# Optimization experiments

Measured on AMD Instinct MI355X. Metric: run time of the kernel, lower is better.

## Reference

```python
import jax, jax.numpy as jnp
import numpy as np

SEQ_LEN, IN_CH, OUT_CH, H, BATCH = 2048, 16, 1, 80, 512


def _lstm(x, W_ih, W_hh, b_ih, b_hh):
    """Single-layer batch-first LSTM (PyTorch gate order i,f,g,o).
    x: [B, T, D]. Returns (outputs [B, T, H], last hidden [B, H])."""
    B = x.shape[0]
    h0 = jnp.zeros((B, H), x.dtype)
    c0 = jnp.zeros((B, H), x.dtype)
    # Precompute input projections for all timesteps in one GEMM: [T, B, 4H]
    xproj = jnp.einsum('btd,gd->tbg', x, W_ih) + (b_ih + b_hh)

    def step(carry, xp_t):
        h, c = carry
        gates = xp_t + h @ W_hh.T  # [B, 4H]
        i, f, g, o = jnp.split(gates, 4, axis=-1)
        i = jax.nn.sigmoid(i)
        f = jax.nn.sigmoid(f)
        g = jnp.tanh(g)
        o = jax.nn.sigmoid(o)
        c = f * c + i * g
        h = o * jnp.tanh(c)
        return (h, c), h

    (h_last, _), hs = jax.lax.scan(step, (h0, c0), xproj)
    return jnp.swapaxes(hs, 0, 1), h_last


def setup_inputs() -> dict:
    key = jax.random.key(0)
    ks = jax.random.split(key, 12)
    s1 = 1.0 / np.sqrt(H)
    d = {
        'x': jax.random.normal(ks[0], (BATCH, SEQ_LEN, IN_CH), jnp.float32),
        'W_ih1': jax.random.uniform(ks[1], (4 * H, IN_CH), jnp.float32, -s1, s1),
        'W_hh1': jax.random.uniform(ks[2], (4 * H, H), jnp.float32, -s1, s1),
        'b_ih1': jax.random.uniform(ks[3], (4 * H,), jnp.float32, -s1, s1),
        'b_hh1': jax.random.uniform(ks[4], (4 * H,), jnp.float32, -s1, s1),
        'W_ih2': jax.random.uniform(ks[5], (4 * H, H), jnp.float32, -s1, s1),
        'W_hh2': jax.random.uniform(ks[6], (4 * H, H), jnp.float32, -s1, s1),
        'b_ih2': jax.random.uniform(ks[7], (4 * H,), jnp.float32, -s1, s1),
        'b_hh2': jax.random.uniform(ks[8], (4 * H,), jnp.float32, -s1, s1),
        'W_d': jax.random.uniform(ks[9], (OUT_CH, H), jnp.float32, -s1, s1),
        'b_d': jax.random.uniform(ks[10], (OUT_CH,), jnp.float32, -s1, s1),
    }
    return d


def reference(x, W_ih1, W_hh1, b_ih1, b_hh1, W_ih2, W_hh2, b_ih2, b_hh2, W_d, b_d):
    B = x.shape[0]
    x = x.reshape((B, SEQ_LEN, IN_CH))
    y1, _ = _lstm(x, W_ih1, W_hh1, b_ih1, b_hh1)          # [B, T, H]
    _, h_last = _lstm(y1, W_ih2, W_hh2, b_ih2, b_hh2)     # [B, H]
    return h_last @ W_d.T + b_d                           # [B, OUT_CH]
```

## Files before the change

### kernel.cpp

```cpp
#include <hip/hip_runtime.h>

#define T_SEQ 2048
#define DIN   16
#define HH    80
#define NTHR  512
#define NBLK  256
#define BT    2
#define ROWE  192

#define L2E   1.44269504088896340736f

typedef _Float16 f16x8 __attribute__((ext_vector_type(8)));
typedef float    f32x4 __attribute__((ext_vector_type(4)));

__device__ __forceinline__ float rcp_fast(float x){ return __builtin_amdgcn_rcpf(x); }
__device__ __forceinline__ float ex2(float x){
#if __has_builtin(__builtin_amdgcn_exp2f)
    return __builtin_amdgcn_exp2f(x);
#else
    return exp2f(x);
#endif
}

#define MF(av, bv, cv) __builtin_amdgcn_mfma_f32_16x16x32_f16(av, bv, cv, 0, 0, 0)

#define L1SLOT(acc, s) { acc = MF(A[s][0], BL0, BIAS[s]); acc = MF(A[s][1], BL1, acc); \
                         acc = MF(A[s][2], BL2, acc); }
#define L2SLOT(acc, s) { acc = MF(A[s][0], BM0, BIAS[s]); acc = MF(A[s][1], BM1, acc); \
                         acc = MF(A[s][2], BM2, acc); acc = MF(A[s][3], BM3, acc); \
                         acc = MF(A[s][4], BM4, acc); }

__global__
__attribute__((amdgpu_flat_work_group_size(NTHR, NTHR)))
__attribute__((amdgpu_waves_per_eu(2, 2)))
void lstm2_mfma(
    const float* __restrict__ x,
    const float* __restrict__ W_ih1, const float* __restrict__ W_hh1,
    const float* __restrict__ b_ih1, const float* __restrict__ b_hh1,
    const float* __restrict__ W_ih2, const float* __restrict__ W_hh2,
    const float* __restrict__ b_ih2, const float* __restrict__ b_hh2,
    const float* __restrict__ W_d,   const float* __restrict__ b_d,
    float* __restrict__ out)
{
    __shared__ __align__(16) _Float16 HB[2][BT][ROWE];

    const int t    = threadIdx.x;
    const int lane = t & 63;
    const int wv   = t >> 6;
    const int m16  = lane & 15;
    const int kgrp = lane >> 4;
    const int b0   = blockIdx.x * BT;

    const int nL1 = (wv < 4) ? 3 : 2;
    const int l1b = (wv < 4) ? 3*wv : 12 + 2*(wv-4);
    const int l2b = (wv < 4) ? 2*wv :  8 + 3*(wv-4);

    f16x8 A[5][5];
    f32x4 BIAS[5];
    {
        const int g  = m16 & 3;
        const int ut = m16 >> 2;
        const float sc = (g == 2) ? (2.f*L2E) : L2E;
        #pragma unroll
        for (int s = 0; s < 5; ++s) {
            const bool sl1 = (s < nL1);
            const int  gt  = sl1 ? (l1b + s) : (l2b + (s - nL1));
            const int  grow = g*HH + 4*gt + ut;
            #pragma unroll
            for (int c = 0; c < 5; ++c) {
                if (sl1 && c >= 3) continue;
                f16x8 a;
                #pragma unroll
                for (int j = 0; j < 8; ++j) {
                    const int k = 32*c + 8*kgrp + j;
                    const float v = sl1
                        ? ((k < DIN) ? W_ih1[grow*DIN + k] : W_hh1[grow*HH + (k - DIN)])
                        : ((k < HH)  ? W_ih2[grow*HH  + k] : W_hh2[grow*HH + (k - HH)]);
                    a[j] = (_Float16)(v * sc);
                }
                A[s][c] = a;
            }
            const int u = 4*gt + kgrp;
            const float* bI = sl1 ? b_ih1 : b_ih2;
            const float* bH = sl1 ? b_hh1 : b_hh2;
            f32x4 bb;
            bb[0] = (bI[       u] + bH[       u]) * L2E;
            bb[1] = (bI[ 80  + u] + bH[ 80  + u]) * L2E;
            bb[2] = (bI[160  + u] + bH[160  + u]) * (2.f*L2E);
            bb[3] = (bI[240  + u] + bH[240  + u]) * L2E;
            BIAS[s] = bb;
        }
    }

    const int  te      = m16 >> 1;
    const bool act_ep  = (m16 < 10);
    const int  sE      = act_ep ? te : 0;
    const bool eL1     = (sE < nL1);
    const int  gtE     = eL1 ? (l1b + sE) : (l2b + (sE - nL1));
    const int  unit_ep = 4*gtE + kgrp;
    const int  seg     = eL1 ? DIN : (DIN + HH);
    const int  batch_ep = lane & 1;

    for (int i = t; i < 2*BT*ROWE; i += NTHR) ((_Float16*)HB)[i] = (_Float16)0.f;
    __syncthreads();

    const int xbn = (lane >> 4) & 1;
    const int xch = lane & 15;
    const float* xptr = x + ((size_t)(b0 + xbn) * T_SEQ) * DIN + xch;
    float xa = 0.f, xbv = 0.f, xcv = 0.f;
    if (wv == 0 && lane < 32) {
        HB[0][xbn][xch] = (_Float16)xptr[0];
        xa  = xptr[1*DIN];
        xbv = xptr[2*DIN];
        xcv = xptr[3*DIN];
    }
    __syncthreads();

    float cst = 0.f;

    #pragma unroll 1
    for (int k = 0; k <= T_SEQ; ++k) {
        const int pb = k & 1, nb = pb ^ 1;

        if (wv == 0 && lane < 32) {
            HB[nb][xbn][xch] = (_Float16)xa;
            xa = xbv; xbv = xcv;
            const int tn = (k + 4 < T_SEQ) ? (k + 4) : (T_SEQ - 1);
            xcv = xptr[(size_t)tn * DIN];
        }

        const _Float16* rb = &HB[pb][lane & 1][0];
        const f16x8 BL0 = *(const f16x8*)(rb +       8*kgrp);
        const f16x8 BL1 = *(const f16x8*)(rb +  32 + 8*kgrp);
        const f16x8 BL2 = *(const f16x8*)(rb +  64 + 8*kgrp);
        const f16x8 BM0 = *(const f16x8*)(rb +  16 + 8*kgrp);
        const f16x8 BM1 = *(const f16x8*)(rb +  48 + 8*kgrp);
        const f16x8 BM2 = *(const f16x8*)(rb +  80 + 8*kgrp);
        const f16x8 BM3 = *(const f16x8*)(rb + 112 + 8*kgrp);
        const f16x8 BM4 = *(const f16x8*)(rb + 144 + 8*kgrp);

        f32x4 acc0, acc1, acc2, acc3, acc4;
        if (wv < 4) {
            L1SLOT(acc0, 0) L1SLOT(acc1, 1) L1SLOT(acc2, 2)
            L2SLOT(acc3, 3) L2SLOT(acc4, 4)
        } else {
            L1SLOT(acc0, 0) L1SLOT(acc1, 1)
            L2SLOT(acc2, 2) L2SLOT(acc3, 3) L2SLOT(acc4, 4)
        }

        float M0 = acc0[0], M1 = acc0[1], M2 = acc0[2], M3 = acc0[3];
        if (te == 1) { M0 = acc1[0]; M1 = acc1[1]; M2 = acc1[2]; M3 = acc1[3]; }
        if (te == 2) { M0 = acc2[0]; M1 = acc2[1]; M2 = acc2[2]; M3 = acc2[3]; }
        if (te == 3) { M0 = acc3[0]; M1 = acc3[1]; M2 = acc3[2]; M3 = acc3[3]; }
        if (te == 4) { M0 = acc4[0]; M1 = acc4[1]; M2 = acc4[2]; M3 = acc4[3]; }

        const float iv = rcp_fast(1.f + ex2(-M0));
        const float fv = rcp_fast(1.f + ex2(-M1));
        const float gv = 1.f - 2.f*rcp_fast(1.f + ex2(M2));
        const float ov = rcp_fast(1.f + ex2(-M3));
        const bool  cup = eL1 || (k > 0);
        if (cup) cst = fv*cst + iv*gv;
        const float tc = 1.f - 2.f*rcp_fast(1.f + ex2(cst * (2.f*L2E)));
        if (act_ep && cup)
            HB[nb][batch_ep][seg + unit_ep] = (_Float16)(ov * tc);

        __syncthreads();
    }

    if (wv == 0) {
        float a0 = 0.f, a1 = 0.f;
        for (int u = lane; u < HH; u += 64) {
            const float wd = W_d[u];
            a0 += wd * (float)HB[1][0][DIN + HH + u];
            a1 += wd * (float)HB[1][1][DIN + HH + u];
        }
        #pragma unroll
        for (int off = 32; off > 0; off >>= 1) {
            a0 += __shfl_down(a0, off);
            a1 += __shfl_down(a1, off);
        }
        if (lane == 0) { out[b0] = a0 + b_d[0]; out[b0 + 1] = a1 + b_d[0]; }
    }
}

extern "C" void kernel_launch(void* const* d_in, const int* in_sizes, int n_in,
                              void* d_out, int out_size, void* d_ws, size_t ws_size,
                              hipStream_t stream) {
    const float* x     = (const float*)d_in[0];
    const float* W_ih1 = (const float*)d_in[1];
    const float* W_hh1 = (const float*)d_in[2];
    const float* b_ih1 = (const float*)d_in[3];
    const float* b_hh1 = (const float*)d_in[4];
    const float* W_ih2 = (const float*)d_in[5];
    const float* W_hh2 = (const float*)d_in[6];
    const float* b_ih2 = (const float*)d_in[7];
    const float* b_hh2 = (const float*)d_in[8];
    const float* W_d   = (const float*)d_in[9];
    const float* b_d   = (const float*)d_in[10];

    lstm2_mfma<<<NBLK, NTHR, 0, stream>>>(x, W_ih1, W_hh1, b_ih1, b_hh1,
                                          W_ih2, W_hh2, b_ih2, b_hh2,
                                          W_d, b_d, (float*)d_out);
}
```

Before: 1.346 ms.

## Split layer 1 onto dot2 VALU waves and layer 2 onto MFMA waves

Layer 1 now runs on three waves using packed fp16 dot2 instructions, with two lanes per hidden unit and a DPP lane swap to combine the halves. Layer 2 runs on four MFMA-only waves, and one wave is left idle. Input x moves to its own shared buffer, so the hidden-state row shrinks and the MFMA waves no longer waste work on padded layer-1 tiles. The aim is to overlap VALU and MFMA work per step and shorten the critical path, at the cost of uneven wave load and heavy register pinning.

```diff
diff --git a/kernel.cpp b/kernel.cpp
--- a/kernel.cpp
+++ b/kernel.cpp
@@ -6,12 +6,13 @@
 #define NTHR  512
 #define NBLK  256
 #define BT    2
-#define ROWE  192
+#define ROWE  160
 
 #define L2E   1.44269504088896340736f
 
 typedef _Float16 f16x8 __attribute__((ext_vector_type(8)));
 typedef float    f32x4 __attribute__((ext_vector_type(4)));
+typedef _Float16 h2v   __attribute__((ext_vector_type(2)));
 
 __device__ __forceinline__ float rcp_fast(float x){ return __builtin_amdgcn_rcpf(x); }
 __device__ __forceinline__ float ex2(float x){
@@ -22,18 +23,35 @@
 #endif
 }
 
+static __device__ __forceinline__ float fdot2f(float w, float h, float acc) {
+    return __builtin_amdgcn_fdot2(__builtin_bit_cast(h2v, w), __builtin_bit_cast(h2v, h), acc, false);
+}
+static __device__ __forceinline__ float pk2(float a, float b) {
+    h2v v; v[0] = (_Float16)a; v[1] = (_Float16)b;
+    return __builtin_bit_cast(float, v);
+}
+static __device__ __forceinline__ float4 pkf4(float4 a, float4 b, float sc){
+    return make_float4(pk2(a.x*sc,a.y*sc), pk2(a.z*sc,a.w*sc),
+                       pk2(b.x*sc,b.y*sc), pk2(b.z*sc,b.w*sc));
+}
+static __device__ __forceinline__ float qswap1(float v){
+    int r = __builtin_amdgcn_update_dpp(0, __builtin_bit_cast(int, v), 0xB1, 0xF, 0xF, true);
+    return __builtin_bit_cast(float, r);
+}
+
 #define MF(av, bv, cv) __builtin_amdgcn_mfma_f32_16x16x32_f16(av, bv, cv, 0, 0, 0)
-
-#define L1SLOT(acc, s) { acc = MF(A[s][0], BL0, BIAS[s]); acc = MF(A[s][1], BL1, acc); \
-                         acc = MF(A[s][2], BL2, acc); }
-#define L2SLOT(acc, s) { acc = MF(A[s][0], BM0, BIAS[s]); acc = MF(A[s][1], BM1, acc); \
-                         acc = MF(A[s][2], BM2, acc); acc = MF(A[s][3], BM3, acc); \
-                         acc = MF(A[s][4], BM4, acc); }
+#define AF(i) __builtin_bit_cast(f16x8, P[i])
+#define L2SLOT(acc, s) { acc = MF(AF(s*5+0), BM0, Q[s]); acc = MF(AF(s*5+1), BM1, acc); \
+                         acc = MF(AF(s*5+2), BM2, acc); acc = MF(AF(s*5+3), BM3, acc); \
+                         acc = MF(AF(s*5+4), BM4, acc); }
+#define DG4(acc, Wq, Hq) { acc = fdot2f(Wq.x, Hq.x, acc); acc = fdot2f(Wq.y, Hq.y, acc); \
+                           acc = fdot2f(Wq.z, Hq.z, acc); acc = fdot2f(Wq.w, Hq.w, acc); }
+#define PIN4(v) asm volatile("" : "+v"(v.x), "+v"(v.y), "+v"(v.z), "+v"(v.w))
 
 __global__
 __attribute__((amdgpu_flat_work_group_size(NTHR, NTHR)))
 __attribute__((amdgpu_waves_per_eu(2, 2)))
-void lstm2_mfma(
+void lstm2_hyb(
     const float* __restrict__ x,
     const float* __restrict__ W_ih1, const float* __restrict__ W_hh1,
     const float* __restrict__ b_ih1, const float* __restrict__ b_hh1,
@@ -43,6 +61,7 @@
     float* __restrict__ out)
 {
     __shared__ __align__(16) _Float16 HB[2][BT][ROWE];
+    __shared__ __align__(16) _Float16 XB[2][BT][DIN];
 
     const int t    = threadIdx.x;
     const int lane = t & 63;
@@ -51,119 +70,146 @@
     const int kgrp = lane >> 4;
     const int b0   = blockIdx.x * BT;
 
-    const int nL1 = (wv < 4) ? 3 : 2;
-    const int l1b = (wv < 4) ? 3*wv : 12 + 2*(wv-4);
-    const int l2b = (wv < 4) ? 2*wv :  8 + 3*(wv-4);
-
-    f16x8 A[5][5];
-    f32x4 BIAS[5];
-    {
+    const int  idx   = (wv << 6) | lane;
+    const int  uL    = idx >> 1;
+    const int  sL    = idx & 1;
+    const bool actL  = (wv < 3) && (idx < 160);
+
+    float4 P[25];
+    f32x4  Q[5];
+
+    if (actL) {
+        #pragma unroll
+        for (int g = 0; g < 4; ++g) {
+            const float sc = (g == 2) ? (2.f*L2E) : L2E;
+            const int grow = g*HH + uL;
+            const float4* Ph = (const float4*)(W_hh1 + (size_t)grow*HH + 40*sL);
+            #pragma unroll
+            for (int c = 0; c < 5; ++c) P[g*6 + c] = pkf4(Ph[2*c], Ph[2*c+1], sc);
+            const float4* Px = (const float4*)(W_ih1 + (size_t)grow*DIN + 8*sL);
+            P[g*6 + 5] = pkf4(Px[0], Px[1], sc);
+            Q[0][g] = (b_ih1[grow] + b_hh1[grow]) * sc;
+        }
+    } else if (wv >= 4) {
+        const int uloc = 20*(wv - 4);
         const int g  = m16 & 3;
         const int ut = m16 >> 2;
         const float sc = (g == 2) ? (2.f*L2E) : L2E;
         #pragma unroll
         for (int s = 0; s < 5; ++s) {
-            const bool sl1 = (s < nL1);
-            const int  gt  = sl1 ? (l1b + s) : (l2b + (s - nL1));
-            const int  grow = g*HH + 4*gt + ut;
+            const int grow = g*HH + (uloc + 4*s + ut);
             #pragma unroll
             for (int c = 0; c < 5; ++c) {
-                if (sl1 && c >= 3) continue;
                 f16x8 a;
                 #pragma unroll
                 for (int j = 0; j < 8; ++j) {
-                    const int k = 32*c + 8*kgrp + j;
-                    const float v = sl1
-                        ? ((k < DIN) ? W_ih1[grow*DIN + k] : W_hh1[grow*HH + (k - DIN)])
-                        : ((k < HH)  ? W_ih2[grow*HH  + k] : W_hh2[grow*HH + (k - HH)]);
+                    const int kk = 32*c + 8*kgrp + j;
+                    const float v = (kk < HH) ? W_ih2[(size_t)grow*HH + kk]
+                                              : W_hh2[(size_t)grow*HH + (kk - HH)];
                     a[j] = (_Float16)(v * sc);
                 }
-                A[s][c] = a;
+                P[s*5 + c] = __builtin_bit_cast(float4, a);
             }
-            const int u = 4*gt + kgrp;
-            const float* bI = sl1 ? b_ih1 : b_ih2;
-            const float* bH = sl1 ? b_hh1 : b_hh2;
-            f32x4 bb;
-            bb[0] = (bI[       u] + bH[       u]) * L2E;
-            bb[1] = (bI[ 80  + u] + bH[ 80  + u]) * L2E;
-            bb[2] = (bI[160  + u] + bH[160  + u]) * (2.f*L2E);
-            bb[3] = (bI[240  + u] + bH[240  + u]) * L2E;
-            BIAS[s] = bb;
-        }
-    }
-
+            const int u = uloc + 4*s + kgrp;
+            Q[s][0] = (b_ih2[       u] + b_hh2[       u]) * L2E;
+            Q[s][1] = (b_ih2[  HH + u] + b_hh2[  HH + u]) * L2E;
+            Q[s][2] = (b_ih2[2*HH + u] + b_hh2[2*HH + u]) * (2.f*L2E);
+            Q[s][3] = (b_ih2[3*HH + u] + b_hh2[3*HH + u]) * L2E;
+        }
+    }
+
+    const int  uloc2   = (wv >= 4) ? 20*(wv - 4) : 0;
     const int  te      = m16 >> 1;
     const bool act_ep  = (m16 < 10);
-    const int  sE      = act_ep ? te : 0;
-    const bool eL1     = (sE < nL1);
-    const int  gtE     = eL1 ? (l1b + sE) : (l2b + (sE - nL1));
-    const int  unit_ep = 4*gtE + kgrp;
-    const int  seg     = eL1 ? DIN : (DIN + HH);
+    const int  unit_ep = uloc2 + 4*(act_ep ? te : 0) + kgrp;
     const int  batch_ep = lane & 1;
 
     for (int i = t; i < 2*BT*ROWE; i += NTHR) ((_Float16*)HB)[i] = (_Float16)0.f;
-    __syncthreads();
-
-    const int xbn = (lane >> 4) & 1;
-    const int xch = lane & 15;
+
+    const int  xbn = (lane - 32) >> 4;
+    const int  xch = lane & 15;
     const float* xptr = x + ((size_t)(b0 + xbn) * T_SEQ) * DIN + xch;
     float xa = 0.f, xbv = 0.f, xcv = 0.f;
-    if (wv == 0 && lane < 32) {
-        HB[0][xbn][xch] = (_Float16)xptr[0];
+    if (wv == 2 && lane >= 32) {
+        XB[0][xbn][xch] = (_Float16)xptr[0];
         xa  = xptr[1*DIN];
         xbv = xptr[2*DIN];
         xcv = xptr[3*DIN];
     }
     __syncthreads();
 
-    float cst = 0.f;
+    float cA = 0.f, cB = 0.f;
 
     #pragma unroll 1
     for (int k = 0; k <= T_SEQ; ++k) {
         const int pb = k & 1, nb = pb ^ 1;
 
-        if (wv == 0 && lane < 32) {
-            HB[nb][xbn][xch] = (_Float16)xa;
+        if (wv == 2 && lane >= 32) {
+            XB[nb][xbn][xch] = (_Float16)xa;
             xa = xbv; xbv = xcv;
             const int tn = (k + 4 < T_SEQ) ? (k + 4) : (T_SEQ - 1);
             xcv = xptr[(size_t)tn * DIN];
         }
 
-        const _Float16* rb = &HB[pb][lane & 1][0];
-        const f16x8 BL0 = *(const f16x8*)(rb +       8*kgrp);
-        const f16x8 BL1 = *(const f16x8*)(rb +  32 + 8*kgrp);
-        const f16x8 BL2 = *(const f16x8*)(rb +  64 + 8*kgrp);
-        const f16x8 BM0 = *(const f16x8*)(rb +  16 + 8*kgrp);
-        const f16x8 BM1 = *(const f16x8*)(rb +  48 + 8*kgrp);
-        const f16x8 BM2 = *(const f16x8*)(rb +  80 + 8*kgrp);
-        const f16x8 BM3 = *(const f16x8*)(rb + 112 + 8*kgrp);
-        const f16x8 BM4 = *(const f16x8*)(rb + 144 + 8*kgrp);
-
-        f32x4 acc0, acc1, acc2, acc3, acc4;
-        if (wv < 4) {
-            L1SLOT(acc0, 0) L1SLOT(acc1, 1) L1SLOT(acc2, 2)
-            L2SLOT(acc3, 3) L2SLOT(acc4, 4)
-        } else {
-            L1SLOT(acc0, 0) L1SLOT(acc1, 1)
-            L2SLOT(acc2, 2) L2SLOT(acc3, 3) L2SLOT(acc4, 4)
-        }
-
-        float M0 = acc0[0], M1 = acc0[1], M2 = acc0[2], M3 = acc0[3];
-        if (te == 1) { M0 = acc1[0]; M1 = acc1[1]; M2 = acc1[2]; M3 = acc1[3]; }
-        if (te == 2) { M0 = acc2[0]; M1 = acc2[1]; M2 = acc2[2]; M3 = acc2[3]; }
-        if (te == 3) { M0 = acc3[0]; M1 = acc3[1]; M2 = acc3[2]; M3 = acc3[3]; }
-        if (te == 4) { M0 = acc4[0]; M1 = acc4[1]; M2 = acc4[2]; M3 = acc4[3]; }
-
-        const float iv = rcp_fast(1.f + ex2(-M0));
-        const float fv = rcp_fast(1.f + ex2(-M1));
-        const float gv = 1.f - 2.f*rcp_fast(1.f + ex2(M2));
-        const float ov = rcp_fast(1.f + ex2(-M3));
-        const bool  cup = eL1 || (k > 0);
-        if (cup) cst = fv*cst + iv*gv;
-        const float tc = 1.f - 2.f*rcp_fast(1.f + ex2(cst * (2.f*L2E)));
-        if (act_ep && cup)
-            HB[nb][batch_ep][seg + unit_ep] = (_Float16)(ov * tc);
-
+        if (wv < 3) {
+            if (k < T_SEQ && idx < 160) {
+                PIN4(P[0]);  PIN4(P[1]);  PIN4(P[2]);  PIN4(P[3]);  PIN4(P[4]);  PIN4(P[5]);
+                PIN4(P[6]);  PIN4(P[7]);  PIN4(P[8]);  PIN4(P[9]);  PIN4(P[10]); PIN4(P[11]);
+                PIN4(P[12]); PIN4(P[13]); PIN4(P[14]); PIN4(P[15]); PIN4(P[16]); PIN4(P[17]);
+                PIN4(P[18]); PIN4(P[19]); PIN4(P[20]); PIN4(P[21]); PIN4(P[22]); PIN4(P[23]);
+                #pragma unroll
+                for (int b = 0; b < BT; ++b) {
+                    const _Float16* hb = &HB[pb][b][40*sL];
+                    const float4 h0 = ((const float4*)hb)[0], h1 = ((const float4*)hb)[1],
+                                 h2 = ((const float4*)hb)[2], h3 = ((const float4*)hb)[3],
+                                 h4 = ((const float4*)hb)[4];
+                    const float4 xv = *(const float4*)(&XB[pb][b][8*sL]);
+                    float ai=0.f, af=0.f, ag=0.f, ao=0.f;
+                    DG4(ai,P[0],h0)  DG4(ai,P[1],h1)  DG4(ai,P[2],h2)  DG4(ai,P[3],h3)  DG4(ai,P[4],h4)  DG4(ai,P[5],xv)
+                    DG4(af,P[6],h0)  DG4(af,P[7],h1)  DG4(af,P[8],h2)  DG4(af,P[9],h3)  DG4(af,P[10],h4) DG4(af,P[11],xv)
+                    DG4(ag,P[12],h0) DG4(ag,P[13],h1) DG4(ag,P[14],h2) DG4(ag,P[15],h3) DG4(ag,P[16],h4) DG4(ag,P[17],xv)
+                    DG4(ao,P[18],h0) DG4(ao,P[19],h1) DG4(ao,P[20],h2) DG4(ao,P[21],h3) DG4(ao,P[22],h4) DG4(ao,P[23],xv)
+                    ai += qswap1(ai); af += qswap1(af); ag += qswap1(ag); ao += qswap1(ao);
+                    if (sL == 0) {
+                        float& cs = b ? cB : cA;
+                        const float iv = rcp_fast(1.f + ex2(-(ai + Q[0][0])));
+                        const float fv = rcp_fast(1.f + ex2(-(af + Q[0][1])));
+                        const float gv = 1.f - 2.f*rcp_fast(1.f + ex2(ag + Q[0][2]));
+                        const float ov = rcp_fast(1.f + ex2(-(ao + Q[0][3])));
+                        cs = fv*cs + iv*gv;
+                        const float tc = 1.f - 2.f*rcp_fast(1.f + ex2(cs * (2.f*L2E)));
+                        HB[nb][b][uL] = (_Float16)(ov * tc);
+                    }
+                }
+            }
+        } else if (wv >= 4) {
+            if (k >= 1) {
+                const _Float16* rb = &HB[pb][lane & 1][0];
+                const f16x8 BM0 = *(const f16x8*)(rb +       8*kgrp);
+                const f16x8 BM1 = *(const f16x8*)(rb +  32 + 8*kgrp);
+                const f16x8 BM2 = *(const f16x8*)(rb +  64 + 8*kgrp);
+                const f16x8 BM3 = *(const f16x8*)(rb +  96 + 8*kgrp);
+                const f16x8 BM4 = *(const f16x8*)(rb + 128 + 8*kgrp);
+                f32x4 acc0, acc1, acc2, acc3, acc4;
+                L2SLOT(acc0, 0) L2SLOT(acc1, 1) L2SLOT(acc2, 2)
+                L2SLOT(acc3, 3) L2SLOT(acc4, 4)
+
+                float M0 = acc0[0], M1 = acc0[1], M2 = acc0[2], M3 = acc0[3];
+                if (te == 1) { M0 = acc1[0]; M1 = acc1[1]; M2 = acc1[2]; M3 = acc1[3]; }
+                if (te == 2) { M0 = acc2[0]; M1 = acc2[1]; M2 = acc2[2]; M3 = acc2[3]; }
+                if (te == 3) { M0 = acc3[0]; M1 = acc3[1]; M2 = acc3[2]; M3 = acc3[3]; }
+                if (te == 4) { M0 = acc4[0]; M1 = acc4[1]; M2 = acc4[2]; M3 = acc4[3]; }
+
+                const float iv = rcp_fast(1.f + ex2(-M0));
+                const float fv = rcp_fast(1.f + ex2(-M1));
+                const float gv = 1.f - 2.f*rcp_fast(1.f + ex2(M2));
+                const float ov = rcp_fast(1.f + ex2(-M3));
+                cA = fv*cA + iv*gv;
+                const float tc = 1.f - 2.f*rcp_fast(1.f + ex2(cA * (2.f*L2E)));
+                if (act_ep)
+                    HB[nb][batch_ep][HH + unit_ep] = (_Float16)(ov * tc);
+            }
+        }
         __syncthreads();
     }
 
@@ -171,8 +217,8 @@
         float a0 = 0.f, a1 = 0.f;
         for (int u = lane; u < HH; u += 64) {
             const float wd = W_d[u];
-            a0 += wd * (float)HB[1][0][DIN + HH + u];
-            a1 += wd * (float)HB[1][1][DIN + HH + u];
+            a0 += wd * (float)HB[1][0][HH + u];
+            a1 += wd * (float)HB[1][1][HH + u];
         }
         #pragma unroll
         for (int off = 32; off > 0; off >>= 1) {
@@ -198,7 +244,7 @@
     const float* W_d   = (const float*)d_in[9];
     const float* b_d   = (const float*)d_in[10];
 
-    lstm2_mfma<<<NBLK, NTHR, 0, stream>>>(x, W_ih1, W_hh1, b_ih1, b_hh1,
-                                          W_ih2, W_hh2, b_ih2, b_hh2,
-                                          W_d, b_d, (float*)d_out);
-}
+    lstm2_hyb<<<NBLK, NTHR, 0, stream>>>(x, W_ih1, W_hh1, b_ih1, b_hh1,
+                                         W_ih2, W_hh2, b_ih2, b_hh2,
+                                         W_d, b_d, (float*)d_out);
+}
```

After: 1.912 ms. 42.0% more time.

## Split waves by layer and stage input sequence in shared-memory ring buffer

Applied to the files above, without the earlier changes.

Waves are reassigned so waves 0-3 compute only layer 1 and waves 4-7 only layer 2, each owning 20 hidden units, instead of mixing layer-1 and layer-2 slots in every wave. Input x is staged in 128-timestep chunks into a 512-entry fp16 shared ring buffer with prefetch, replacing the per-step single-wave global load into the hidden buffer. The hidden row layout shrinks because x is no longer stored in it. Layer-1 waves now issue 15 MFMAs and layer-2 waves 25 per step, so the per-step critical path may be set by the layer-2 waves, and the added shared memory may matter.

```diff
diff --git a/kernel.cpp b/kernel.cpp
--- a/kernel.cpp
+++ b/kernel.cpp
@@ -6,7 +6,9 @@
 #define NTHR  512
 #define NBLK  256
 #define BT    2
-#define ROWE  192
+#define ROWE  160
+#define XRT   512
+#define XCH   128
 
 #define L2E   1.44269504088896340736f
 
@@ -23,12 +25,11 @@
 }
 
 #define MF(av, bv, cv) __builtin_amdgcn_mfma_f32_16x16x32_f16(av, bv, cv, 0, 0, 0)
-
-#define L1SLOT(acc, s) { acc = MF(A[s][0], BL0, BIAS[s]); acc = MF(A[s][1], BL1, acc); \
-                         acc = MF(A[s][2], BL2, acc); }
-#define L2SLOT(acc, s) { acc = MF(A[s][0], BM0, BIAS[s]); acc = MF(A[s][1], BM1, acc); \
-                         acc = MF(A[s][2], BM2, acc); acc = MF(A[s][3], BM3, acc); \
-                         acc = MF(A[s][4], BM4, acc); }
+#define L1SLOT(acc, s) { acc = MF(A[s][0], B0, Q[s]); acc = MF(A[s][1], B1, acc); \
+                         acc = MF(A[s][2], B2, acc); }
+#define L2SLOT(acc, s) { acc = MF(A[s][0], B0, Q[s]); acc = MF(A[s][1], B1, acc); \
+                         acc = MF(A[s][2], B2, acc); acc = MF(A[s][3], B3, acc); \
+                         acc = MF(A[s][4], B4, acc); }
 
 __global__
 __attribute__((amdgpu_flat_work_group_size(NTHR, NTHR)))
@@ -43,127 +44,137 @@
     float* __restrict__ out)
 {
     __shared__ __align__(16) _Float16 HB[2][BT][ROWE];
+    __shared__ __align__(16) _Float16 XR[XRT][BT][DIN];
 
     const int t    = threadIdx.x;
     const int lane = t & 63;
     const int wv   = t >> 6;
+    const bool isL1w = (wv < 4);
     const int m16  = lane & 15;
     const int kgrp = lane >> 4;
     const int b0   = blockIdx.x * BT;
 
-    const int nL1 = (wv < 4) ? 3 : 2;
-    const int l1b = (wv < 4) ? 3*wv : 12 + 2*(wv-4);
-    const int l2b = (wv < 4) ? 2*wv :  8 + 3*(wv-4);
+    const int uloc = isL1w ? 20*wv : 20*(wv-4);
 
     f16x8 A[5][5];
-    f32x4 BIAS[5];
+    f32x4 Q[5];
     {
         const int g  = m16 & 3;
         const int ut = m16 >> 2;
         const float sc = (g == 2) ? (2.f*L2E) : L2E;
         #pragma unroll
         for (int s = 0; s < 5; ++s) {
-            const bool sl1 = (s < nL1);
-            const int  gt  = sl1 ? (l1b + s) : (l2b + (s - nL1));
-            const int  grow = g*HH + 4*gt + ut;
+            const int grow = g*HH + (uloc + 4*s + ut);
             #pragma unroll
             for (int c = 0; c < 5; ++c) {
-                if (sl1 && c >= 3) continue;
+                if (isL1w && c >= 3) continue;
                 f16x8 a;
                 #pragma unroll
                 for (int j = 0; j < 8; ++j) {
-                    const int k = 32*c + 8*kgrp + j;
-                    const float v = sl1
-                        ? ((k < DIN) ? W_ih1[grow*DIN + k] : W_hh1[grow*HH + (k - DIN)])
-                        : ((k < HH)  ? W_ih2[grow*HH  + k] : W_hh2[grow*HH + (k - HH)]);
+                    const int kk = 32*c + 8*kgrp + j;
+                    const float v = isL1w
+                        ? ((kk < DIN) ? W_ih1[(size_t)grow*DIN + kk]
+                                      : W_hh1[(size_t)grow*HH + (kk - DIN)])
+                        : ((kk < HH)  ? W_ih2[(size_t)grow*HH + kk]
+                                      : W_hh2[(size_t)grow*HH + (kk - HH)]);
                     a[j] = (_Float16)(v * sc);
                 }
                 A[s][c] = a;
             }
-            const int u = 4*gt + kgrp;
-            const float* bI = sl1 ? b_ih1 : b_ih2;
-            const float* bH = sl1 ? b_hh1 : b_hh2;
+            const int u = uloc + 4*s + kgrp;
+            const float* bI = isL1w ? b_ih1 : b_ih2;
+            const float* bH = isL1w ? b_hh1 : b_hh2;
             f32x4 bb;
             bb[0] = (bI[       u] + bH[       u]) * L2E;
-            bb[1] = (bI[ 80  + u] + bH[ 80  + u]) * L2E;
-            bb[2] = (bI[160  + u] + bH[160  + u]) * (2.f*L2E);
-            bb[3] = (bI[240  + u] + bH[240  + u]) * L2E;
-            BIAS[s] = bb;
+            bb[1] = (bI[  HH + u] + bH[  HH + u]) * L2E;
+            bb[2] = (bI[2*HH + u] + bH[2*HH + u]) * (2.f*L2E);
+            bb[3] = (bI[3*HH + u] + bH[3*HH + u]) * L2E;
+            Q[s] = bb;
         }
     }
 
     const int  te      = m16 >> 1;
     const bool act_ep  = (m16 < 10);
-    const int  sE      = act_ep ? te : 0;
-    const bool eL1     = (sE < nL1);
-    const int  gtE     = eL1 ? (l1b + sE) : (l2b + (sE - nL1));
-    const int  unit_ep = 4*gtE + kgrp;
-    const int  seg     = eL1 ? DIN : (DIN + HH);
+    const int  unit_ep = uloc + 4*(act_ep ? te : 0) + kgrp;
+    const int  seg     = isL1w ? 0 : HH;
     const int  batch_ep = lane & 1;
 
     for (int i = t; i < 2*BT*ROWE; i += NTHR) ((_Float16*)HB)[i] = (_Float16)0.f;
+
+    const int toff = t >> 2, xb = (t >> 1) & 1, c8 = t & 1;
+    const float* xsrc = x + ((size_t)(b0 + xb) * T_SEQ) * DIN + c8*8;
+    #pragma unroll
+    for (int c0 = 0; c0 < 2*XCH; c0 += XCH) {
+        const int tt = c0 + toff;
+        const float4 va = *(const float4*)(xsrc + (size_t)tt * DIN);
+        const float4 vb = *(const float4*)(xsrc + (size_t)tt * DIN + 4);
+        f16x8 h;
+        h[0]=(_Float16)va.x; h[1]=(_Float16)va.y; h[2]=(_Float16)va.z; h[3]=(_Float16)va.w;
+        h[4]=(_Float16)vb.x; h[5]=(_Float16)vb.y; h[6]=(_Float16)vb.z; h[7]=(_Float16)vb.w;
+        *(f16x8*)&XR[tt][xb][c8*8] = h;
+    }
     __syncthreads();
 
-    const int xbn = (lane >> 4) & 1;
-    const int xch = lane & 15;
-    const float* xptr = x + ((size_t)(b0 + xbn) * T_SEQ) * DIN + xch;
-    float xa = 0.f, xbv = 0.f, xcv = 0.f;
-    if (wv == 0 && lane < 32) {
-        HB[0][xbn][xch] = (_Float16)xptr[0];
-        xa  = xptr[1*DIN];
-        xbv = xptr[2*DIN];
-        xcv = xptr[3*DIN];
-    }
-    __syncthreads();
-
     float cst = 0.f;
+    float4 xva{}, xvb{};
+    int pend_tt = -1;
 
     #pragma unroll 1
     for (int k = 0; k <= T_SEQ; ++k) {
         const int pb = k & 1, nb = pb ^ 1;
 
-        if (wv == 0 && lane < 32) {
-            HB[nb][xbn][xch] = (_Float16)xa;
-            xa = xbv; xbv = xcv;
-            const int tn = (k + 4 < T_SEQ) ? (k + 4) : (T_SEQ - 1);
-            xcv = xptr[(size_t)tn * DIN];
-        }
-
-        const _Float16* rb = &HB[pb][lane & 1][0];
-        const f16x8 BL0 = *(const f16x8*)(rb +       8*kgrp);
-        const f16x8 BL1 = *(const f16x8*)(rb +  32 + 8*kgrp);
-        const f16x8 BL2 = *(const f16x8*)(rb +  64 + 8*kgrp);
-        const f16x8 BM0 = *(const f16x8*)(rb +  16 + 8*kgrp);
-        const f16x8 BM1 = *(const f16x8*)(rb +  48 + 8*kgrp);
-        const f16x8 BM2 = *(const f16x8*)(rb +  80 + 8*kgrp);
-        const f16x8 BM3 = *(const f16x8*)(rb + 112 + 8*kgrp);
-        const f16x8 BM4 = *(const f16x8*)(rb + 144 + 8*kgrp);
-
-        f32x4 acc0, acc1, acc2, acc3, acc4;
-        if (wv < 4) {
-            L1SLOT(acc0, 0) L1SLOT(acc1, 1) L1SLOT(acc2, 2)
-            L2SLOT(acc3, 3) L2SLOT(acc4, 4)
-        } else {
-            L1SLOT(acc0, 0) L1SLOT(acc1, 1)
-            L2SLOT(acc2, 2) L2SLOT(acc3, 3) L2SLOT(acc4, 4)
-        }
-
-        float M0 = acc0[0], M1 = acc0[1], M2 = acc0[2], M3 = acc0[3];
-        if (te == 1) { M0 = acc1[0]; M1 = acc1[1]; M2 = acc1[2]; M3 = acc1[3]; }
-        if (te == 2) { M0 = acc2[0]; M1 = acc2[1]; M2 = acc2[2]; M3 = acc2[3]; }
-        if (te == 3) { M0 = acc3[0]; M1 = acc3[1]; M2 = acc3[2]; M3 = acc3[3]; }
-        if (te == 4) { M0 = acc4[0]; M1 = acc4[1]; M2 = acc4[2]; M3 = acc4[3]; }
-
-        const float iv = rcp_fast(1.f + ex2(-M0));
-        const float fv = rcp_fast(1.f + ex2(-M1));
-        const float gv = 1.f - 2.f*rcp_fast(1.f + ex2(M2));
-        const float ov = rcp_fast(1.f + ex2(-M3));
-        const bool  cup = eL1 || (k > 0);
-        if (cup) cst = fv*cst + iv*gv;
-        const float tc = 1.f - 2.f*rcp_fast(1.f + ex2(cst * (2.f*L2E)));
-        if (act_ep && cup)
-            HB[nb][batch_ep][seg + unit_ep] = (_Float16)(ov * tc);
-
+        if ((k & (XCH-1)) == 0 && (k + 2*XCH + XCH) <= T_SEQ + XCH) {
+            const int tt = k + 2*XCH + toff;
+            if (tt < T_SEQ) {
+                xva = *(const float4*)(xsrc + (size_t)tt * DIN);
+                xvb = *(const float4*)(xsrc + (size_t)tt * DIN + 4);
+                pend_tt = tt;
+            }
+        } else if ((k & (XCH-1)) == 1 && pend_tt >= 0) {
+            f16x8 h;
+            h[0]=(_Float16)xva.x; h[1]=(_Float16)xva.y; h[2]=(_Float16)xva.z; h[3]=(_Float16)xva.w;
+            h[4]=(_Float16)xvb.x; h[5]=(_Float16)xvb.y; h[6]=(_Float16)xvb.z; h[7]=(_Float16)xvb.w;
+            *(f16x8*)&XR[pend_tt & (XRT-1)][xb][c8*8] = h;
+            pend_tt = -1;
+        }
+
+        const bool act = isL1w ? (k < T_SEQ) : (k >= 1);
+        if (act) {
+            const _Float16* hb = &HB[pb][lane & 1][0];
+            f32x4 acc0, acc1, acc2, acc3, acc4;
+            if (isL1w) {
+                const _Float16* xrb = &XR[k & (XRT-1)][lane & 1][0];
+                const _Float16* p0  = (kgrp < 2) ? (xrb + 8*kgrp) : (hb + 8*kgrp - 16);
+                const f16x8 B0 = *(const f16x8*)p0;
+                const f16x8 B1 = *(const f16x8*)(hb + 16 + 8*kgrp);
+                const f16x8 B2 = *(const f16x8*)(hb + 48 + 8*kgrp);
+                L1SLOT(acc0, 0) L1SLOT(acc1, 1) L1SLOT(acc2, 2)
+                L1SLOT(acc3, 3) L1SLOT(acc4, 4)
+            } else {
+                const f16x8 B0 = *(const f16x8*)(hb +       8*kgrp);
+                const f16x8 B1 = *(const f16x8*)(hb +  32 + 8*kgrp);
+                const f16x8 B2 = *(const f16x8*)(hb +  64 + 8*kgrp);
+                const f16x8 B3 = *(const f16x8*)(hb +  96 + 8*kgrp);
+                const f16x8 B4 = *(const f16x8*)(hb + 128 + 8*kgrp);
+                L2SLOT(acc0, 0) L2SLOT(acc1, 1) L2SLOT(acc2, 2)
+                L2SLOT(acc3, 3) L2SLOT(acc4, 4)
+            }
+
+            float M0 = acc0[0], M1 = acc0[1], M2 = acc0[2], M3 = acc0[3];
+            if (te == 1) { M0 = acc1[0]; M1 = acc1[1]; M2 = acc1[2]; M3 = acc1[3]; }
+            if (te == 2) { M0 = acc2[0]; M1 = acc2[1]; M2 = acc2[2]; M3 = acc2[3]; }
+            if (te == 3) { M0 = acc3[0]; M1 = acc3[1]; M2 = acc3[2]; M3 = acc3[3]; }
+            if (te == 4) { M0 = acc4[0]; M1 = acc4[1]; M2 = acc4[2]; M3 = acc4[3]; }
+
+            const float iv = rcp_fast(1.f + ex2(-M0));
+            const float fv = rcp_fast(1.f + ex2(-M1));
+            const float gv = 1.f - 2.f*rcp_fast(1.f + ex2(M2));
+            const float ov = rcp_fast(1.f + ex2(-M3));
+            cst = fv*cst + iv*gv;
+            const float tc = 1.f - 2.f*rcp_fast(1.f + ex2(cst * (2.f*L2E)));
+            if (act_ep)
+                HB[nb][batch_ep][seg + unit_ep] = (_Float16)(ov * tc);
+        }
         __syncthreads();
     }
 
@@ -171,8 +182,8 @@
         float a0 = 0.f, a1 = 0.f;
         for (int u = lane; u < HH; u += 64) {
             const float wd = W_d[u];
-            a0 += wd * (float)HB[1][0][DIN + HH + u];
-            a1 += wd * (float)HB[1][1][DIN + HH + u];
+            a0 += wd * (float)HB[1][0][HH + u];
+            a1 += wd * (float)HB[1][1][HH + u];
         }
         #pragma unroll
         for (int off = 32; off > 0; off >>= 1) {
```

After: 1.459 ms. 1.08x slower.
